# Performance work log

Hardware: AMD Instinct MI355X
Metric: run time of the kernel (lower is better)

The kernel has to match this reference:

```python
import jax, jax.numpy as jnp
import numpy as np

B, T, IN, H, L, OUT = 2048, 512, 4, 64, 4, 5


def setup_inputs() -> dict:
    key = jax.random.key(0)
    ks = jax.random.split(key, 9)
    s = 0.1  # keep gates out of saturation
    return {
        "x": jax.random.normal(ks[0], (B, T, IN), jnp.float32),
        "W_ih0": jax.random.normal(ks[1], (4 * H, IN), jnp.float32) * s,
        "W_ih_r": jax.random.normal(ks[2], (L - 1, 4 * H, H), jnp.float32) * s,
        "W_hh": jax.random.normal(ks[3], (L, 4 * H, H), jnp.float32) * s,
        "b_ih": jax.random.normal(ks[4], (L, 4 * H), jnp.float32) * s,
        "b_hh": jax.random.normal(ks[5], (L, 4 * H), jnp.float32) * s,
        "W_fc": jax.random.normal(ks[6], (OUT, H), jnp.float32) * s,
        "b_fc": jax.random.normal(ks[7], (OUT,), jnp.float32) * s,
    }


def _lstm_layer(xs, W_ih, W_hh, b_ih, b_hh):
    # xs: [B, T, D_in] -> hs: [B, T, H]. PyTorch gate order: i, f, g, o.
    b, t = xs.shape[0], xs.shape[1]
    h_dim = W_hh.shape[1]
    # Precompute input contribution for all timesteps (one big GEMM).
    xg = jnp.einsum('btd,gd->btg', xs, W_ih) + b_ih  # [B, T, 4H]

    def step(carry, xg_t):
        h, c = carry
        g = xg_t + h @ W_hh.T + b_hh  # [B, 4H]
        i, f, gg, o = jnp.split(g, 4, axis=-1)
        c = jax.nn.sigmoid(f) * c + jax.nn.sigmoid(i) * jnp.tanh(gg)
        h = jax.nn.sigmoid(o) * jnp.tanh(c)
        return (h, c), h

    init = (jnp.zeros((b, h_dim), xs.dtype), jnp.zeros((b, h_dim), xs.dtype))
    (_, _), hs = jax.lax.scan(step, init, jnp.swapaxes(xg, 0, 1))  # hs: [T, B, H]
    return jnp.swapaxes(hs, 0, 1)


def reference(x, W_ih0, W_ih_r, W_hh, b_ih, b_hh, W_fc, b_fc):
    hs = _lstm_layer(x, W_ih0, W_hh[0], b_ih[0], b_hh[0])
    for l in range(1, L):
        hs = _lstm_layer(hs, W_ih_r[l - 1], W_hh[l], b_ih[l], b_hh[l])
    # fc on last timestep of top layer
    return hs[:, -1, :] @ W_fc.T + b_fc  # [B, OUT]
```

## Files before the change

kernel.cpp:

```cpp
#include <hip/hip_runtime.h>


#define B_    2048
#define T_    512
#define H_    64
#define OUT_  5
#define LOG2E 1.44269504088896340736f

typedef _Float16 f16;
typedef __attribute__((ext_vector_type(4))) _Float16 f16x4;
typedef __attribute__((ext_vector_type(8))) _Float16 f16x8;
typedef __attribute__((ext_vector_type(4))) float f32x4;
typedef __attribute__((ext_vector_type(2))) unsigned long long u64x2;

__device__ __forceinline__ float rcpf(float v) { return __builtin_amdgcn_rcpf(v); }
__device__ __forceinline__ float ex2(float v)  { return __builtin_amdgcn_exp2f(v); }

__global__ __launch_bounds__(1024, 4) void lstm_ring7_k(
    const float* __restrict__ x,
    const float* __restrict__ W_ih0,
    const float* __restrict__ W_ihr,
    const float* __restrict__ W_hh,
    const float* __restrict__ b_ih,
    const float* __restrict__ b_hh,
    const float* __restrict__ W_fc,
    const float* __restrict__ b_fc,
    float* __restrict__ out)
{
    const int tid  = threadIdx.x;
    const int wave = tid >> 6;
    const int l    = wave >> 2;
    const int jj   = wave & 3;
    const int lane = tid & 63;
    const int q    = lane >> 4;
    const int ln   = lane & 15;
    const int b0   = blockIdx.x * 8;

    __shared__ f16  hbuf[4][4][1024];
    __shared__ f16  xlds[T_][8][4];
    __shared__ float hf[8][H_ + 1];
    __shared__ int  flg[16];

    for (int k = tid; k < 8192; k += 1024) ((unsigned*)hbuf)[k] = 0u;
    if (tid < 16) flg[tid] = 0;

#pragma unroll
    for (int k = 0; k < 4; ++k) {
        const int idx = tid + k * 1024;
        const int bb  = idx >> 9, tt = idx & 511;
        const float4 v = *(const float4*)(x + (size_t)(b0 + bb) * (T_ * 4) + tt * 4);
        f16x4 h4; h4[0] = (f16)v.x; h4[1] = (f16)v.y; h4[2] = (f16)v.z; h4[3] = (f16)v.w;
        *(f16x4*)&xlds[tt][bb][0] = h4;
    }

    const float* Whh = W_hh + (size_t)l * 256 * 64;
    const float* Wih = (l == 0) ? W_ih0 : (W_ihr + (size_t)(l - 1) * 256 * 64);
    const float scg[4] = {-LOG2E, -LOG2E, 2.0f * LOG2E, -LOG2E};

    f16x8 Wf[4][4];
    f32x4 Cb[4];
#pragma unroll
    for (int g4 = 0; g4 < 4; ++g4) {
        const int n = g4 * 64 + jj * 16 + ln;
        const float bv = (b_ih[l * 256 + n] + b_hh[l * 256 + n]) * scg[g4];
        Cb[g4][0] = bv; Cb[g4][1] = bv; Cb[g4][2] = bv; Cb[g4][3] = bv;
#pragma unroll
        for (int kt = 0; kt < 4; ++kt) {
            f16x8 f;
#pragma unroll
            for (int e = 0; e < 8; ++e) {
                float wv;
                if (kt < 2)      wv = Whh[n * 64 + kt * 32 + q * 8 + e];
                else if (l == 0) wv = (kt == 2 && q == 0 && e < 4) ? Wih[n * 4 + e] : 0.0f;
                else             wv = Wih[n * 64 + (kt - 2) * 32 + q * 8 + e];
                f[e] = (f16)(wv * scg[g4]);
            }
            Wf[g4][kt] = f;
        }
    }

    const int swz   = (ln & 7) << 4;
    const int roffA = (ln * 128 + q * 16) ^ swz;
    const int roffB = (ln * 128 + 64 + q * 16) ^ swz;
    char* ownB      = (char*)&hbuf[l][0][0];
    const char* prvB = (const char*)&hbuf[(l > 0) ? (l - 1) : 0][0][0];

    int woff[2];
#pragma unroll
    for (int rr = 0; rr < 2; ++rr) {
        const int r = 4 * q + rr;
        woff[rr] = (r * 128 + (jj * 16 + ln) * 2) ^ ((r & 7) << 4);
    }
    const int  xb  = 2 * (ln >> 2) + (ln & 1);
    const bool xok = (q == 0) && ((ln & 3) < 2);

    const bool fU1 = (l > 0) && (lane < 4);
    const int  fI1 = fU1 ? (4 * (l - 1) + lane) : 0;
    int fI2 = 0, fO2 = 0; bool fU2 = false;
    if (lane < 3)                { fI2 = 4 * l + ((jj + 1 + lane) & 3); fO2 = 0;  fU2 = true; }
    else if (lane < 7 && l < 3)  { fI2 = 4 * (l + 1) + (lane - 3);      fO2 = -3; fU2 = true; }

    __syncthreads();

    float cst[2] = {0.f, 0.f};
    const float K2 = 2.0f * LOG2E;

    auto body = [&](const int t, const int sl, const int sn) {
        f32x4 acc[4];
        if (l > 0) {
            unsigned g = 0;
            for (;;) {
                int v = 0x7fffffff;
                if (fU1) v = __hip_atomic_load(&flg[fI1], __ATOMIC_ACQUIRE,
                                               __HIP_MEMORY_SCOPE_WORKGROUP);
                if (__all(v >= t + 1)) break;
                if (++g > 2) __builtin_amdgcn_s_sleep(1);
                if (g > (1u << 16)) break;
            }
            const char* ri = prvB + sn * 2048;
            const f16x8 A2 = *(const f16x8*)(ri + roffA);
            const f16x8 A3 = *(const f16x8*)(ri + roffB);
#pragma unroll
            for (int g4 = 0; g4 < 4; ++g4)
                acc[g4] = __builtin_amdgcn_mfma_f32_16x16x32_f16(A2, Wf[g4][2], Cb[g4], 0, 0, 0);
#pragma unroll
            for (int g4 = 0; g4 < 4; ++g4)
                acc[g4] = __builtin_amdgcn_mfma_f32_16x16x32_f16(A3, Wf[g4][3], acc[g4], 0, 0, 0);
        } else {
            unsigned long long xw = 0ull;
            if (xok) xw = *(const unsigned long long*)&xlds[t][xb][0];
            u64x2 tmp; tmp[0] = xw; tmp[1] = 0ull;
            const f16x8 A2 = __builtin_bit_cast(f16x8, tmp);
#pragma unroll
            for (int g4 = 0; g4 < 4; ++g4)
                acc[g4] = __builtin_amdgcn_mfma_f32_16x16x32_f16(A2, Wf[g4][2], Cb[g4], 0, 0, 0);
        }

        {
            unsigned g = 0;
            for (;;) {
                int v = 0x7fffffff;
                if (fU2) v = __hip_atomic_load(&flg[fI2], __ATOMIC_ACQUIRE,
                                               __HIP_MEMORY_SCOPE_WORKGROUP);
                if (__all(v >= t + fO2)) break;
                if (++g > 2) __builtin_amdgcn_s_sleep(1);
                if (g > (1u << 16)) break;
            }
        }
        const char* ro = ownB + sl * 2048;
        const f16x8 A0 = *(const f16x8*)(ro + roffA);
        const f16x8 A1 = *(const f16x8*)(ro + roffB);
        __builtin_amdgcn_s_setprio(1);
#pragma unroll
        for (int g4 = 0; g4 < 4; ++g4)
            acc[g4] = __builtin_amdgcn_mfma_f32_16x16x32_f16(A0, Wf[g4][0], acc[g4], 0, 0, 0);
#pragma unroll
        for (int g4 = 0; g4 < 4; ++g4)
            acc[g4] = __builtin_amdgcn_mfma_f32_16x16x32_f16(A1, Wf[g4][1], acc[g4], 0, 0, 0);
        __builtin_amdgcn_s_setprio(0);

        char* wr = ownB + sn * 2048;
#pragma unroll
        for (int rr = 0; rr < 2; ++rr) {
            const float Ei = ex2(acc[0][rr]);
            const float Ef = ex2(acc[1][rr]);
            const float Eg = ex2(acc[2][rr]);
            const float Eo = ex2(acc[3][rr]);
            const float sf   = rcpf(1.0f + Ef);
            const float di   = (1.0f + Ei) * (1.0f + Eg);
            const float sitg = fmaf(Eg, K2, -K2) * rcpf(di);
            const float Cp   = fmaf(sf, cst[rr], sitg);
            cst[rr] = Cp;
            const float Ec = ex2(Cp);
            const float dc = (1.0f + Eo) * (1.0f + Ec);
            const float h  = (Ec - 1.0f) * rcpf(dc);
            *(f16*)(wr + woff[rr]) = (f16)h;
            if (l == 3 && t == T_ - 1) hf[2 * q + rr][jj * 16 + ln] = h;
        }

        if (lane == 0)
            __hip_atomic_store(&flg[wave], t + 1, __ATOMIC_RELEASE,
                               __HIP_MEMORY_SCOPE_WORKGROUP);
    };

#pragma unroll 1
    for (int t = 0; t < T_; t += 4) {
        body(t,     0, 1);
        body(t + 1, 1, 2);
        body(t + 2, 2, 3);
        body(t + 3, 3, 0);
    }

    __syncthreads();
    if (tid < 8 * OUT_) {
        const int b = tid / OUT_, o = tid % OUT_;
        float a = b_fc[o];
#pragma unroll
        for (int k = 0; k < H_; ++k)
            a = fmaf(hf[b][k], W_fc[o * H_ + k], a);
        out[(b0 + b) * OUT_ + o] = a;
    }
}

extern "C" void kernel_launch(void* const* d_in, const int* in_sizes, int n_in,
                              void* d_out, int out_size, void* d_ws, size_t ws_size,
                              hipStream_t stream) {
    const float* x     = (const float*)d_in[0];
    const float* W_ih0 = (const float*)d_in[1];
    const float* W_ihr = (const float*)d_in[2];
    const float* W_hh  = (const float*)d_in[3];
    const float* b_ih  = (const float*)d_in[4];
    const float* b_hh  = (const float*)d_in[5];
    const float* W_fc  = (const float*)d_in[6];
    const float* b_fc  = (const float*)d_in[7];
    float* out = (float*)d_out;

    lstm_ring7_k<<<dim3(B_ / 8), dim3(1024), 0, stream>>>(
        x, W_ih0, W_ihr, W_hh, b_ih, b_hh, W_fc, b_fc, out);
}
```

Baseline: 566.4 us.

## Batch input-projection MFMAs for two timesteps using spare MFMA rows

The input projection (previous layer's h or x) for two consecutive timesteps is now packed into the unused rows of a single MFMA pass, done on even steps. Odd steps then only run the recurrent W_hh MFMAs on the accumulator lanes that already hold their input contribution, using remapped row offsets. This roughly halves the input-side MFMA work and one wait on the previous layer per step pair. In exchange, layers now wait for the previous layer to be two steps ahead, which adds pipeline skew. It also relies on more intricate row mapping and a changed poll threshold, which raises the risk of correctness errors.

```diff
diff --git a/kernel.cpp b/kernel.cpp
--- a/kernel.cpp
+++ b/kernel.cpp
@@ -16,7 +16,7 @@
 __device__ __forceinline__ float rcpf(float v) { return __builtin_amdgcn_rcpf(v); }
 __device__ __forceinline__ float ex2(float v)  { return __builtin_amdgcn_exp2f(v); }
 
-__global__ __launch_bounds__(1024, 4) void lstm_ring7_k(
+__global__ __launch_bounds__(1024, 4) void lstm_ring9_k(
     const float* __restrict__ x,
     const float* __restrict__ W_ih0,
     const float* __restrict__ W_ihr,
@@ -82,6 +82,15 @@
     const int swz   = (ln & 7) << 4;
     const int roffA = (ln * 128 + q * 16) ^ swz;
     const int roffB = (ln * 128 + 64 + q * 16) ^ swz;
+    const int lnx   = ln ^ 2;
+    const int swzx  = (lnx & 7) << 4;
+    const int roffAx = (lnx * 128 + q * 16) ^ swzx;
+    const int roffBx = (lnx * 128 + 64 + q * 16) ^ swzx;
+    const int srcrow = 4 * (ln >> 2) + (ln & 1);
+    const int swz2   = (srcrow & 7) << 4;
+    const int roffA2 = (srcrow * 128 + q * 16) ^ swz2;
+    const int roffB2 = (srcrow * 128 + 64 + q * 16) ^ swz2;
+    const int tsel   = (ln >> 1) & 1;
     char* ownB      = (char*)&hbuf[l][0][0];
     const char* prvB = (const char*)&hbuf[(l > 0) ? (l - 1) : 0][0][0];
 
@@ -91,8 +100,8 @@
         const int r = 4 * q + rr;
         woff[rr] = (r * 128 + (jj * 16 + ln) * 2) ^ ((r & 7) << 4);
     }
-    const int  xb  = 2 * (ln >> 2) + (ln & 1);
-    const bool xok = (q == 0) && ((ln & 3) < 2);
+    const int  xb2 = 2 * (ln >> 2) + (ln & 1);
+    const bool xok = (lane < 16);
 
     const bool fU1 = (l > 0) && (lane < 4);
     const int  fI1 = fU1 ? (4 * (l - 1) + lane) : 0;
@@ -105,67 +114,15 @@
     float cst[2] = {0.f, 0.f};
     const float K2 = 2.0f * LOG2E;
 
-    auto body = [&](const int t, const int sl, const int sn) {
-        f32x4 acc[4];
-        if (l > 0) {
-            unsigned g = 0;
-            for (;;) {
-                int v = 0x7fffffff;
-                if (fU1) v = __hip_atomic_load(&flg[fI1], __ATOMIC_ACQUIRE,
-                                               __HIP_MEMORY_SCOPE_WORKGROUP);
-                if (__all(v >= t + 1)) break;
-                if (++g > 2) __builtin_amdgcn_s_sleep(1);
-                if (g > (1u << 16)) break;
-            }
-            const char* ri = prvB + sn * 2048;
-            const f16x8 A2 = *(const f16x8*)(ri + roffA);
-            const f16x8 A3 = *(const f16x8*)(ri + roffB);
-#pragma unroll
-            for (int g4 = 0; g4 < 4; ++g4)
-                acc[g4] = __builtin_amdgcn_mfma_f32_16x16x32_f16(A2, Wf[g4][2], Cb[g4], 0, 0, 0);
-#pragma unroll
-            for (int g4 = 0; g4 < 4; ++g4)
-                acc[g4] = __builtin_amdgcn_mfma_f32_16x16x32_f16(A3, Wf[g4][3], acc[g4], 0, 0, 0);
-        } else {
-            unsigned long long xw = 0ull;
-            if (xok) xw = *(const unsigned long long*)&xlds[t][xb][0];
-            u64x2 tmp; tmp[0] = xw; tmp[1] = 0ull;
-            const f16x8 A2 = __builtin_bit_cast(f16x8, tmp);
-#pragma unroll
-            for (int g4 = 0; g4 < 4; ++g4)
-                acc[g4] = __builtin_amdgcn_mfma_f32_16x16x32_f16(A2, Wf[g4][2], Cb[g4], 0, 0, 0);
-        }
-
-        {
-            unsigned g = 0;
-            for (;;) {
-                int v = 0x7fffffff;
-                if (fU2) v = __hip_atomic_load(&flg[fI2], __ATOMIC_ACQUIRE,
-                                               __HIP_MEMORY_SCOPE_WORKGROUP);
-                if (__all(v >= t + fO2)) break;
-                if (++g > 2) __builtin_amdgcn_s_sleep(1);
-                if (g > (1u << 16)) break;
-            }
-        }
-        const char* ro = ownB + sl * 2048;
-        const f16x8 A0 = *(const f16x8*)(ro + roffA);
-        const f16x8 A1 = *(const f16x8*)(ro + roffB);
-        __builtin_amdgcn_s_setprio(1);
-#pragma unroll
-        for (int g4 = 0; g4 < 4; ++g4)
-            acc[g4] = __builtin_amdgcn_mfma_f32_16x16x32_f16(A0, Wf[g4][0], acc[g4], 0, 0, 0);
-#pragma unroll
-        for (int g4 = 0; g4 < 4; ++g4)
-            acc[g4] = __builtin_amdgcn_mfma_f32_16x16x32_f16(A1, Wf[g4][1], acc[g4], 0, 0, 0);
-        __builtin_amdgcn_s_setprio(0);
-
+    auto pointwise = [&](const int t, const int sn, f32x4 (&acc)[4], const int ra) {
         char* wr = ownB + sn * 2048;
 #pragma unroll
         for (int rr = 0; rr < 2; ++rr) {
-            const float Ei = ex2(acc[0][rr]);
-            const float Ef = ex2(acc[1][rr]);
-            const float Eg = ex2(acc[2][rr]);
-            const float Eo = ex2(acc[3][rr]);
+            const int rg = ra + rr;
+            const float Ei = ex2(acc[0][rg]);
+            const float Ef = ex2(acc[1][rg]);
+            const float Eg = ex2(acc[2][rg]);
+            const float Eo = ex2(acc[3][rg]);
             const float sf   = rcpf(1.0f + Ef);
             const float di   = (1.0f + Ei) * (1.0f + Eg);
             const float sitg = fmaf(Eg, K2, -K2) * rcpf(di);
@@ -177,18 +134,97 @@
             *(f16*)(wr + woff[rr]) = (f16)h;
             if (l == 3 && t == T_ - 1) hf[2 * q + rr][jj * 16 + ln] = h;
         }
-
+    };
+
+    auto partner_poll = [&](const int t) {
+        unsigned g = 0;
+        for (;;) {
+            int v = 0x7fffffff;
+            if (fU2) v = __hip_atomic_load(&flg[fI2], __ATOMIC_ACQUIRE,
+                                           __HIP_MEMORY_SCOPE_WORKGROUP);
+            if (__all(v >= t + fO2)) break;
+            if (++g > 2) __builtin_amdgcn_s_sleep(1);
+            if (g > (1u << 16)) break;
+        }
+    };
+
+    auto release = [&](const int t) {
         if (lane == 0)
             __hip_atomic_store(&flg[wave], t + 1, __ATOMIC_RELEASE,
                                __HIP_MEMORY_SCOPE_WORKGROUP);
     };
 
+    auto evenb = [&](const int t, const int sl, const int sn, const int sn2,
+                     f32x4 (&acc)[4]) {
+        if (l > 0) {
+            unsigned g = 0;
+            for (;;) {
+                int v = 0x7fffffff;
+                if (fU1) v = __hip_atomic_load(&flg[fI1], __ATOMIC_ACQUIRE,
+                                               __HIP_MEMORY_SCOPE_WORKGROUP);
+                if (__all(v >= t + 2)) break;
+                if (++g > 2) __builtin_amdgcn_s_sleep(1);
+                if (g > (1u << 16)) break;
+            }
+            const char* ri = prvB + (tsel ? sn2 : sn) * 2048;
+            const f16x8 A2 = *(const f16x8*)(ri + roffA2);
+            const f16x8 A3 = *(const f16x8*)(ri + roffB2);
+#pragma unroll
+            for (int g4 = 0; g4 < 4; ++g4)
+                acc[g4] = __builtin_amdgcn_mfma_f32_16x16x32_f16(A2, Wf[g4][2], Cb[g4], 0, 0, 0);
+#pragma unroll
+            for (int g4 = 0; g4 < 4; ++g4)
+                acc[g4] = __builtin_amdgcn_mfma_f32_16x16x32_f16(A3, Wf[g4][3], acc[g4], 0, 0, 0);
+        } else {
+            unsigned long long xw = 0ull;
+            if (xok) xw = *(const unsigned long long*)&xlds[t + tsel][xb2][0];
+            u64x2 tmp; tmp[0] = xw; tmp[1] = 0ull;
+            const f16x8 A2 = __builtin_bit_cast(f16x8, tmp);
+#pragma unroll
+            for (int g4 = 0; g4 < 4; ++g4)
+                acc[g4] = __builtin_amdgcn_mfma_f32_16x16x32_f16(A2, Wf[g4][2], Cb[g4], 0, 0, 0);
+        }
+
+        partner_poll(t);
+        const char* ro = ownB + sl * 2048;
+        const f16x8 A0 = *(const f16x8*)(ro + roffA);
+        const f16x8 A1 = *(const f16x8*)(ro + roffB);
+        __builtin_amdgcn_s_setprio(1);
+#pragma unroll
+        for (int g4 = 0; g4 < 4; ++g4)
+            acc[g4] = __builtin_amdgcn_mfma_f32_16x16x32_f16(A0, Wf[g4][0], acc[g4], 0, 0, 0);
+#pragma unroll
+        for (int g4 = 0; g4 < 4; ++g4)
+            acc[g4] = __builtin_amdgcn_mfma_f32_16x16x32_f16(A1, Wf[g4][1], acc[g4], 0, 0, 0);
+        pointwise(t, sn, acc, 0);
+        __builtin_amdgcn_s_setprio(0);
+        release(t);
+    };
+
+    auto oddb = [&](const int t, const int sl, const int sn, f32x4 (&acc)[4]) {
+        partner_poll(t);
+        const char* ro = ownB + sl * 2048;
+        const f16x8 A0 = *(const f16x8*)(ro + roffAx);
+        const f16x8 A1 = *(const f16x8*)(ro + roffBx);
+        __builtin_amdgcn_s_setprio(1);
+#pragma unroll
+        for (int g4 = 0; g4 < 4; ++g4)
+            acc[g4] = __builtin_amdgcn_mfma_f32_16x16x32_f16(A0, Wf[g4][0], acc[g4], 0, 0, 0);
+#pragma unroll
+        for (int g4 = 0; g4 < 4; ++g4)
+            acc[g4] = __builtin_amdgcn_mfma_f32_16x16x32_f16(A1, Wf[g4][1], acc[g4], 0, 0, 0);
+        pointwise(t, sn, acc, 2);
+        __builtin_amdgcn_s_setprio(0);
+        release(t);
+    };
+
 #pragma unroll 1
     for (int t = 0; t < T_; t += 4) {
-        body(t,     0, 1);
-        body(t + 1, 1, 2);
-        body(t + 2, 2, 3);
-        body(t + 3, 3, 0);
+        f32x4 acc[4];
+        evenb(t,     0, 1, 2, acc);
+        oddb (t + 1, 1, 2,    acc);
+        evenb(t + 2, 2, 3, 0, acc);
+        oddb (t + 3, 3, 0,    acc);
     }
 
     __syncthreads();
@@ -215,6 +251,6 @@
     const float* b_fc  = (const float*)d_in[7];
     float* out = (float*)d_out;
 
-    lstm_ring7_k<<<dim3(B_ / 8), dim3(1024), 0, stream>>>(
+    lstm_ring9_k<<<dim3(B_ / 8), dim3(1024), 0, stream>>>(
         x, W_ih0, W_ihr, W_hh, b_ih, b_hh, W_fc, b_fc, out);
 }
```

Measured after the change: 498.7 us. 11.9% less time.
